# Kernel optimization log

Measured on AMD Instinct MI355X. Metric: run time of the kernel, lower is better.

The kernel has to match this reference:

```python
import jax, jax.numpy as jnp
import numpy as np

B, N = 4, 512
NF, EF = 12, 1          # node / edge feature dims (fixed in GraphClassifier)
QK = 128                # baseFeatNum -> QKDims = nValDims
NV_D, EV_D = 128, 32    # nValDims, eValDims
TR = 2 * NV_D           # Trans output = nValDims*2 = 256
NCLS = 5
EPS = 1e-5


def setup_inputs() -> dict:
    key = jax.random.key(0)
    ks = jax.random.split(key, 16)
    s = 0.1
    return {
        "nodes": jax.random.normal(ks[0], (B, N, NF), jnp.float32),
        "edges": jax.random.normal(ks[1], (B, N, N, EF), jnp.float32),
        "distances": jax.random.uniform(ks[2], (B, N, N), jnp.float32),
        "mask": jax.random.randint(ks[3], (B, N, N), 0, 2) > 0,
        "Wq": jax.random.normal(ks[4], (QK, NF), jnp.float32) * s,
        "bq": jnp.zeros((QK,), jnp.float32),
        "Wk": jax.random.normal(ks[5], (QK, NF), jnp.float32) * s,
        "bk": jnp.zeros((QK,), jnp.float32),
        "Wnv": jax.random.normal(ks[6], (NV_D, NF), jnp.float32) * s,
        "bnv": jnp.zeros((NV_D,), jnp.float32),
        "Wev": jax.random.normal(ks[7], (EV_D, EF), jnp.float32) * s,
        "bev": jnp.zeros((EV_D,), jnp.float32),
        "Wt": jax.random.normal(ks[8], (TR, NV_D + EV_D), jnp.float32) * s,
        "bt": jnp.zeros((TR,), jnp.float32),
        "gamma": jnp.ones((TR,), jnp.float32),
        "beta": jnp.zeros((TR,), jnp.float32),
        "Wc": jax.random.normal(ks[9], (NCLS, TR), jnp.float32) * s,
        "bc": jnp.zeros((NCLS,), jnp.float32),
    }


def reference(nodes, edges, distances, mask, Wq, bq, Wk, bk, Wnv, bnv,
              Wev, bev, Wt, bt, gamma, beta, Wc, bc):
    coeff = 1.0 / np.sqrt(QK).astype(np.float32)
    Q = nodes @ Wq.T + bq            # (b,N,QK)
    K = nodes @ Wk.T + bk            # (b,N,QK)
    NV = nodes @ Wnv.T + bnv         # (b,N,nValDims); NV[b,i,j]=NV_node[b,j] after repeat
    EV = edges @ Wev.T + bev         # (b,N,N,eValDims)

    dist_w = 1.0 / (distances + 1.0)
    scores = jnp.einsum('bik,bjk->bij', Q, K) * dist_w * coeff
    scores = jnp.where(mask, -jnp.inf, scores)
    w = jax.nn.softmax(scores, axis=-1)
    w = jnp.where(jnp.isnan(w), 0.0, w)  # fully-masked rows -> zero weights

    node_part = jnp.einsum('bij,bjd->bid', w, NV)     # weighted node values
    edge_part = jnp.einsum('bij,bijd->bid', w, EV)    # weighted edge values
    vals = jnp.concatenate([node_part, edge_part], axis=-1)
    vals = jnp.tanh(vals) @ Wt.T + bt                 # (b,N,2*nValDims)

    # BatchNorm1d in training mode: biased batch stats over (b*N)
    flat = vals.reshape(-1, TR)
    mu = flat.mean(axis=0)
    var = flat.var(axis=0)
    flat = (flat - mu) / jnp.sqrt(var + EPS) * gamma + beta
    vals = flat.reshape(vals.shape)

    return vals @ Wc.T + bc                           # (b,N,5)
```

## Files before the change

### kernel.cpp

```cpp
#include <hip/hip_runtime.h>
#include <math.h>

#define NNODE 512
#define NBATCH 4
#define NFEAT 12
#define QKD 128
#define NVD 128
#define EVD 32
#define CATD 160
#define CATB 168
#define TRD 256
#define NCLS 5
#define NROWS 2048
#define EPSV 1e-5f
#define NSTATBUF 8
#define NCHUNK 4
#define JC 128
#define RPB 8
#define SSW 132
#define KBW 136

typedef float floatx4 __attribute__((ext_vector_type(4)));
typedef __bf16 bf16x8 __attribute__((ext_vector_type(8)));
typedef unsigned short ushort_t;
typedef ushort_t ushort8 __attribute__((ext_vector_type(8)));
typedef ushort_t ushort4v __attribute__((ext_vector_type(4)));

static __device__ __forceinline__ ushort_t f2bf(float x) {
  unsigned int u = __float_as_uint(x);
  return (ushort_t)((u + 0x7fffu + ((u >> 16) & 1u)) >> 16);
}
static __device__ __forceinline__ bf16x8 pack8(ushort4v lo, ushort4v hi) {
  ushort8 u;
  u[0] = lo.x; u[1] = lo.y; u[2] = lo.z; u[3] = lo.w;
  u[4] = hi.x; u[5] = hi.y; u[6] = hi.z; u[7] = hi.w;
  return __builtin_bit_cast(bf16x8, u);
}

__global__ __launch_bounds__(256) void qkv_kernel(
    const float* __restrict__ nodes,
    const float* __restrict__ Wq, const float* __restrict__ bq,
    const float* __restrict__ Wk, const float* __restrict__ bk,
    const float* __restrict__ Wnv, const float* __restrict__ bnv,
    const float* __restrict__ Wt,
    ushort_t* __restrict__ Qb, ushort_t* __restrict__ Kb,
    ushort_t* __restrict__ NVT, ushort_t* __restrict__ Wtb,
    float* __restrict__ stats) {
  const int tid = threadIdx.x;
  const int blk = blockIdx.x;
  const int rowbase = blk * 8;
  const int b = rowbase >> 9;
  const int jloc = rowbase & (NNODE - 1);
  if (blk < 2 * NSTATBUF) stats[blk * 256 + tid] = 0.f;
  {
    const int base = blk * 160;
    if (tid < 160) Wtb[base + tid] = f2bf(Wt[base + tid]);
  }
  __shared__ float sn[RPB][NFEAT];
  if (tid < RPB * NFEAT) ((float*)sn)[tid] = nodes[(size_t)rowbase * NFEAT + tid];
  __syncthreads();

  {
    const int d  = tid & 127;
    const int rg = tid >> 7;
    float wq[NFEAT], wk[NFEAT];
#pragma unroll
    for (int k = 0; k < NFEAT; ++k) {
      wq[k] = Wq[d * NFEAT + k];
      wk[k] = Wk[d * NFEAT + k];
    }
    const float bqv = bq[d], bkv = bk[d];
#pragma unroll
    for (int rr = 0; rr < 4; ++rr) {
      const int rl = rg * 4 + rr;
      float aq = bqv, ak = bkv;
#pragma unroll
      for (int k = 0; k < NFEAT; ++k) {
        const float n = sn[rl][k];
        aq = fmaf(n, wq[k], aq);
        ak = fmaf(n, wk[k], ak);
      }
      Qb[(size_t)(rowbase + rl) * QKD + d] = f2bf(aq);
      Kb[(size_t)(rowbase + rl) * QKD + d] = f2bf(ak);
    }
  }
  {
    const int d    = tid >> 1;
    const int half = tid & 1;
    float wnv[NFEAT];
#pragma unroll
    for (int k = 0; k < NFEAT; ++k) wnv[k] = Wnv[d * NFEAT + k];
    const float bnvv = bnv[d];
    ushort4v v;
#pragma unroll
    for (int e = 0; e < 4; ++e) {
      const int rl = half * 4 + e;
      float av = bnvv;
#pragma unroll
      for (int k = 0; k < NFEAT; ++k) av = fmaf(sn[rl][k], wnv[k], av);
      v[e] = f2bf(av);
    }
    *(ushort4v*)(NVT + (size_t)b * QKD * NNODE + (size_t)d * NNODE +
                 jloc + half * 4) = v;
  }
}

__global__ __launch_bounds__(512) void attnTrans_kernel(
    const ushort_t* __restrict__ Qb, const ushort_t* __restrict__ Kb,
    const ushort_t* __restrict__ NVT,
    const float* __restrict__ edges, const float* __restrict__ dist,
    const int* __restrict__ mask,
    const float* __restrict__ Wev, const float* __restrict__ bev,
    const ushort_t* __restrict__ Wtb, const float* __restrict__ bt,
    float* __restrict__ vals, float* __restrict__ stats) {
  __shared__ ushort_t sKB[2][JC * KBW];
  __shared__ ushort_t sNV[2][QKD * KBW];
  __shared__ __align__(16) float sS[16][SSW];
  __shared__ ushort_t catb[RPB * CATB];
  __shared__ float sF[16], sF2[RPB], sSe[RPB], sSw[RPB];

  const int tid = threadIdx.x;
  const int bid = blockIdx.x;
  const int b   = bid >> 6;
  const int rg  = bid & 63;
  const int rowbase = b * NNODE + rg * RPB;

  const int lane = tid & 63;
  const int wv   = tid >> 6;
  const int col  = lane & 15;
  const int kg   = lane >> 4;

  if (tid < 16) sF[tid] = 0.f;

  const int jl  = wv * 16 + col;
  const int dpv = wv * 16 + col;
  const int sd   = tid >> 2;
  const int sseg = (tid & 3) * 32;

  float dd[NCHUNK][4]; int mm[NCHUNK][4];
  float ee0[NCHUNK], ee1[NCHUNK];
#pragma unroll
  for (int c = 0; c < NCHUNK; ++c) {
#pragma unroll
    for (int r = 0; r < 4; ++r) {
      const size_t off =
          (size_t)(rowbase + ((kg * 4 + r) & 7)) * NNODE + c * JC + jl;
      dd[c][r] = dist[off];
      mm[c][r] = mask[off];
    }
    ee0[c] = edges[(size_t)(rowbase + wv) * NNODE + c * JC + lane];
    ee1[c] = edges[(size_t)(rowbase + wv) * NNODE + c * JC + 64 + lane];
  }

  bf16x8 aq[4];
  {
    const ushort_t* Qr = Qb + (size_t)(rowbase + (col & 7)) * QKD;
#pragma unroll
    for (int ks = 0; ks < 4; ++ks)
      aq[ks] = pack8(*(const ushort4v*)(Qr + ks * 32 + kg * 4),
                     *(const ushort4v*)(Qr + ks * 32 + 16 + kg * 4));
  }

  ushort8 kreg[4], nreg[4];
  {
    const ushort8* ksrc =
        (const ushort8*)(Kb + (size_t)(b * NNODE + sd) * QKD + sseg);
    const ushort8* nsrc = (const ushort8*)(NVT + (size_t)b * QKD * NNODE +
                                           (size_t)sd * NNODE + sseg);
#pragma unroll
    for (int t = 0; t < 4; ++t) { kreg[t] = ksrc[t]; nreg[t] = nsrc[t]; }
  }

  float m_run = -__builtin_inff(), l_run = 0.f, se_run = 0.f;
  floatx4 acc = {0.f, 0.f, 0.f, 0.f};
  const float coeff = 0.0883883476483184f;

#pragma unroll
  for (int c = 0; c < NCHUNK; ++c) {
    {
      ushort8* kdst = (ushort8*)(&sKB[c & 1][0] + sd * KBW + sseg);
      ushort8* ndst = (ushort8*)(&sNV[c & 1][0] + sd * KBW + sseg);
#pragma unroll
      for (int t = 0; t < 4; ++t) { kdst[t] = kreg[t]; ndst[t] = nreg[t]; }
    }
    __syncthreads();

    if (c < NCHUNK - 1) {
      const int jb2 = (c + 1) * JC;
      const ushort8* ksrc =
          (const ushort8*)(Kb + (size_t)(b * NNODE + jb2 + sd) * QKD + sseg);
      const ushort8* nsrc = (const ushort8*)(NVT + (size_t)b * QKD * NNODE +
                                             (size_t)sd * NNODE + jb2 + sseg);
#pragma unroll
      for (int t = 0; t < 4; ++t) { kreg[t] = ksrc[t]; nreg[t] = nsrc[t]; }
    }

    {
      floatx4 sc = {0.f, 0.f, 0.f, 0.f};
      const ushort_t* kb = &sKB[c & 1][0] + (size_t)jl * KBW;
#pragma unroll
      for (int ks = 0; ks < 4; ++ks) {
        const bf16x8 bfk = pack8(*(const ushort4v*)(kb + ks * 32 + kg * 4),
                                 *(const ushort4v*)(kb + ks * 32 + 16 + kg * 4));
        sc = __builtin_amdgcn_mfma_f32_16x16x32_bf16(aq[ks], bfk, sc, 0, 0, 0);
      }
#pragma unroll
      for (int r = 0; r < 4; ++r) {
        float s = sc[r] * coeff / (dd[c][r] + 1.0f);
        if (mm[c][r]) s = -__builtin_inff();
        sS[kg * 4 + r][jl] = s;
      }
    }
    __syncthreads();

    {
      const float v0 = sS[wv][lane];
      const float v1 = sS[wv][lane + 64];
      float mc = fmaxf(v0, v1);
#pragma unroll
      for (int s = 1; s < 64; s <<= 1) mc = fmaxf(mc, __shfl_xor(mc, s, 64));
      const float mn = fmaxf(m_run, mc);
      const float f = (m_run > -__builtin_inff()) ? __expf(m_run - mn) : 0.f;
      float w0 = 0.f, w1 = 0.f;
      if (mn > -__builtin_inff()) {
        w0 = __expf(v0 - mn);
        w1 = __expf(v1 - mn);
      }
      sS[wv][lane]      = w0;
      sS[wv][lane + 64] = w1;
      float lc = w0 + w1;
      float sec = fmaf(w0, ee0[c], w1 * ee1[c]);
#pragma unroll
      for (int s = 1; s < 64; s <<= 1) {
        lc  += __shfl_xor(lc, s, 64);
        sec += __shfl_xor(sec, s, 64);
      }
      l_run  = l_run * f + lc;
      se_run = se_run * f + sec;
      m_run  = mn;
      if (lane == 0) sF[wv] = f;
    }
    __syncthreads();

    {
      acc[0] *= sF[kg * 4 + 0];
      acc[1] *= sF[kg * 4 + 1];
      acc[2] *= sF[kg * 4 + 2];
      acc[3] *= sF[kg * 4 + 3];
      const ushort_t* nv = &sNV[c & 1][0] + (size_t)dpv * KBW;
#pragma unroll
      for (int ks = 0; ks < 4; ++ks) {
        const float4 lo = *(const float4*)&sS[col][ks * 32 + kg * 4];
        const float4 hi = *(const float4*)&sS[col][ks * 32 + 16 + kg * 4];
        ushort8 u;
        u[0] = f2bf(lo.x); u[1] = f2bf(lo.y); u[2] = f2bf(lo.z); u[3] = f2bf(lo.w);
        u[4] = f2bf(hi.x); u[5] = f2bf(hi.y); u[6] = f2bf(hi.z); u[7] = f2bf(hi.w);
        const bf16x8 aw = __builtin_bit_cast(bf16x8, u);
        const bf16x8 bnv = pack8(*(const ushort4v*)(nv + ks * 32 + kg * 4),
                                 *(const ushort4v*)(nv + ks * 32 + 16 + kg * 4));
        acc = __builtin_amdgcn_mfma_f32_16x16x32_bf16(aw, bnv, acc, 0, 0, 0);
      }
    }
  }

  {
    const float inv = (l_run > 0.f) ? 1.f / l_run : 0.f;
    if (lane == 0) {
      sF2[wv] = inv;
      sSe[wv] = se_run * inv;
      sSw[wv] = (l_run > 0.f) ? 1.f : 0.f;
    }
  }
  __syncthreads();

  if (kg < 2) {
#pragma unroll
    for (int r = 0; r < 4; ++r) {
      const int row = kg * 4 + r;
      catb[row * CATB + dpv] = f2bf(tanhf(acc[r] * sF2[row]));
    }
  }
  if (tid < RPB * EVD) {
    const int r = tid >> 5, de = tid & 31;
    catb[r * CATB + NVD + de] =
        f2bf(tanhf(fmaf(Wev[de], sSe[r], bev[de] * sSw[r])));
  }
  __syncthreads();

  {
    bf16x8 af[5];
    const ushort_t* cr = catb + (size_t)(col & 7) * CATB;
#pragma unroll
    for (int ks = 0; ks < 5; ++ks)
      af[ks] = pack8(*(const ushort4v*)(cr + ks * 32 + kg * 4),
                     *(const ushort4v*)(cr + ks * 32 + 16 + kg * 4));
    float* sbuf = stats + (size_t)(bid & (NSTATBUF - 1)) * 2 * TRD;
#pragma unroll
    for (int t = 0; t < 2; ++t) {
      const int o = (wv * 2 + t) * 16 + col;
      const ushort_t* wr = Wtb + (size_t)o * CATD;
      floatx4 a2 = {0.f, 0.f, 0.f, 0.f};
#pragma unroll
      for (int ks = 0; ks < 5; ++ks) {
        const bf16x8 bf = pack8(*(const ushort4v*)(wr + ks * 32 + kg * 4),
                                *(const ushort4v*)(wr + ks * 32 + 16 + kg * 4));
        a2 = __builtin_amdgcn_mfma_f32_16x16x32_bf16(af[ks], bf, a2, 0, 0, 0);
      }
      const float bto = bt[o];
      float s1 = 0.f, s2 = 0.f;
#pragma unroll
      for (int r = 0; r < 4; ++r) {
        const float v2 = a2[r] + bto;
        if (kg < 2) {
          vals[(size_t)(rowbase + kg * 4 + r) * TRD + o] = v2;
          s1 += v2;
          s2 = fmaf(v2, v2, s2);
        }
      }
      s1 += __shfl_xor(s1, 16, 64); s2 += __shfl_xor(s2, 16, 64);
      s1 += __shfl_xor(s1, 32, 64); s2 += __shfl_xor(s2, 32, 64);
      if (kg == 0) {
        atomicAdd(&sbuf[o], s1);
        atomicAdd(&sbuf[TRD + o], s2);
      }
    }
  }
}

__global__ __launch_bounds__(256) void outbn_kernel(
    const float* __restrict__ vals, const float* __restrict__ stats,
    const float* __restrict__ gamma, const float* __restrict__ beta,
    const float* __restrict__ Wc, const float* __restrict__ bc,
    float* __restrict__ out) {
  __shared__ float sW[NCLS][TRD];
  __shared__ float sb[NCLS];
  __shared__ float red[4][NCLS];
  const int tid = threadIdx.x;
  const int o = tid;
  float s1 = 0.f, s2 = 0.f;
#pragma unroll
  for (int k = 0; k < NSTATBUF; ++k) {
    s1 += stats[k * 2 * TRD + o];
    s2 += stats[k * 2 * TRD + TRD + o];
  }
  const float invN = 1.0f / (float)NROWS;
  const float mu  = s1 * invN;
  const float var = s2 * invN - mu * mu;
  const float inv = 1.0f / sqrtf(var + EPSV);
  const float g = gamma[o] * inv;
  const float bterm = beta[o] - mu * g;
  float v[NCLS];
#pragma unroll
  for (int c = 0; c < NCLS; ++c) {
    const float wc = Wc[c * TRD + o];
    sW[c][o] = wc * g;
    v[c] = wc * bterm;
  }
#pragma unroll
  for (int s = 1; s < 64; s <<= 1) {
#pragma unroll
    for (int c = 0; c < NCLS; ++c) v[c] += __shfl_xor(v[c], s, 64);
  }
  if ((tid & 63) == 0) {
#pragma unroll
    for (int c = 0; c < NCLS; ++c) red[tid >> 6][c] = v[c];
  }
  __syncthreads();
  if (tid < NCLS)
    sb[tid] = bc[tid] + red[0][tid] + red[1][tid] + red[2][tid] + red[3][tid];
  __syncthreads();

  const int lane = tid & 63;
  const int row = blockIdx.x * 4 + (tid >> 6);
  float vv[TRD / 64];
#pragma unroll
  for (int t = 0; t < TRD / 64; ++t)
    vv[t] = vals[(size_t)row * TRD + lane + 64 * t];
#pragma unroll
  for (int c = 0; c < NCLS; ++c) {
    float p = 0.f;
#pragma unroll
    for (int t = 0; t < TRD / 64; ++t)
      p = fmaf(vv[t], sW[c][lane + 64 * t], p);
#pragma unroll
    for (int s = 1; s < 64; s <<= 1) p += __shfl_xor(p, s, 64);
    if (lane == 0) out[(size_t)row * NCLS + c] = p + sb[c];
  }
}

extern "C" void kernel_launch(void* const* d_in, const int* in_sizes, int n_in,
                              void* d_out, int out_size, void* d_ws, size_t ws_size,
                              hipStream_t stream) {
  (void)in_sizes; (void)n_in; (void)out_size; (void)ws_size;
  const float* nodes = (const float*)d_in[0];
  const float* edges = (const float*)d_in[1];
  const float* dist  = (const float*)d_in[2];
  const int*   mask  = (const int*)d_in[3];
  const float* Wq  = (const float*)d_in[4];
  const float* bq  = (const float*)d_in[5];
  const float* Wk  = (const float*)d_in[6];
  const float* bk  = (const float*)d_in[7];
  const float* Wnv = (const float*)d_in[8];
  const float* bnv = (const float*)d_in[9];
  const float* Wev = (const float*)d_in[10];
  const float* bev = (const float*)d_in[11];
  const float* Wt  = (const float*)d_in[12];
  const float* bt  = (const float*)d_in[13];
  const float* gamma = (const float*)d_in[14];
  const float* beta  = (const float*)d_in[15];
  const float* Wc  = (const float*)d_in[16];
  const float* bc  = (const float*)d_in[17];

  char* w = (char*)d_ws;
  ushort_t* Qb  = (ushort_t*)w;                w += (size_t)NROWS * QKD * 2;
  ushort_t* Kb  = (ushort_t*)w;                w += (size_t)NROWS * QKD * 2;
  ushort_t* NVT = (ushort_t*)w;                w += (size_t)NBATCH * QKD * NNODE * 2;
  ushort_t* Wtb = (ushort_t*)w;                w += (size_t)TRD * CATD * 2;
  float* vals  = (float*)w;                    w += (size_t)NROWS * TRD * 4;
  float* stats = (float*)w;
  float* outp  = (float*)d_out;

  qkv_kernel<<<NROWS / RPB, 256, 0, stream>>>(nodes, Wq, bq, Wk, bk, Wnv, bnv,
                                              Wt, Qb, Kb, NVT, Wtb, stats);
  attnTrans_kernel<<<NROWS / RPB, 512, 0, stream>>>(
      Qb, Kb, NVT, edges, dist, mask, Wev, bev, Wtb, bt, vals, stats);
  outbn_kernel<<<NROWS / 4, 256, 0, stream>>>(vals, stats, gamma, beta,
                                              Wc, bc, outp);
}
```

Before: 34.47 us.

## Permute K-dim layout for direct MFMA fragment loads, drop LDS staging of K/NV

```diff
diff --git a/kernel.cpp b/kernel.cpp
--- a/kernel.cpp
+++ b/kernel.cpp
@@ -18,23 +18,22 @@
 #define JC 128
 #define RPB 8
 #define SSW 132
-#define KBW 136
+#define WBW 136
 
 typedef float floatx4 __attribute__((ext_vector_type(4)));
 typedef __bf16 bf16x8 __attribute__((ext_vector_type(8)));
 typedef unsigned short ushort_t;
-typedef ushort_t ushort8 __attribute__((ext_vector_type(8)));
 typedef ushort_t ushort4v __attribute__((ext_vector_type(4)));
 
 static __device__ __forceinline__ ushort_t f2bf(float x) {
   unsigned int u = __float_as_uint(x);
   return (ushort_t)((u + 0x7fffu + ((u >> 16) & 1u)) >> 16);
 }
-static __device__ __forceinline__ bf16x8 pack8(ushort4v lo, ushort4v hi) {
-  ushort8 u;
-  u[0] = lo.x; u[1] = lo.y; u[2] = lo.z; u[3] = lo.w;
-  u[4] = hi.x; u[5] = hi.y; u[6] = hi.z; u[7] = hi.w;
-  return __builtin_bit_cast(bf16x8, u);
+static __device__ __forceinline__ int slot32(int r) {
+  return ((r & 15) >> 2) * 8 + (r & 3) + ((r >> 4) << 2);
+}
+static __device__ __forceinline__ int kslot(int k) {
+  return (k & ~31) + slot32(k & 31);
 }
 
 __global__ __launch_bounds__(256) void qkv_kernel(
@@ -52,10 +51,8 @@
   const int b = rowbase >> 9;
   const int jloc = rowbase & (NNODE - 1);
   if (blk < 2 * NSTATBUF) stats[blk * 256 + tid] = 0.f;
-  {
-    const int base = blk * 160;
-    if (tid < 160) Wtb[base + tid] = f2bf(Wt[base + tid]);
-  }
+  if (tid < CATD)
+    Wtb[(size_t)blk * CATD + kslot(tid)] = f2bf(Wt[(size_t)blk * CATD + tid]);
   __shared__ float sn[RPB][NFEAT];
   if (tid < RPB * NFEAT) ((float*)sn)[tid] = nodes[(size_t)rowbase * NFEAT + tid];
   __syncthreads();
@@ -63,6 +60,7 @@
   {
     const int d  = tid & 127;
     const int rg = tid >> 7;
+    const int sd = kslot(d);
     float wq[NFEAT], wk[NFEAT];
 #pragma unroll
     for (int k = 0; k < NFEAT; ++k) {
@@ -80,8 +78,8 @@
         aq = fmaf(n, wq[k], aq);
         ak = fmaf(n, wk[k], ak);
       }
-      Qb[(size_t)(rowbase + rl) * QKD + d] = f2bf(aq);
-      Kb[(size_t)(rowbase + rl) * QKD + d] = f2bf(ak);
+      Qb[(size_t)(rowbase + rl) * QKD + sd] = f2bf(aq);
+      Kb[(size_t)(rowbase + rl) * QKD + sd] = f2bf(ak);
     }
   }
   {
@@ -100,8 +98,9 @@
       for (int k = 0; k < NFEAT; ++k) av = fmaf(sn[rl][k], wnv[k], av);
       v[e] = f2bf(av);
     }
-    *(ushort4v*)(NVT + (size_t)b * QKD * NNODE + (size_t)d * NNODE +
-                 jloc + half * 4) = v;
+    const int js = jloc + half * 4;
+    const int jsl = (js & ~31) + slot32(js & 31);
+    *(ushort4v*)(NVT + (size_t)b * QKD * NNODE + (size_t)d * NNODE + jsl) = v;
   }
 }
 
@@ -113,10 +112,9 @@
     const float* __restrict__ Wev, const float* __restrict__ bev,
     const ushort_t* __restrict__ Wtb, const float* __restrict__ bt,
     float* __restrict__ vals, float* __restrict__ stats) {
-  __shared__ ushort_t sKB[2][JC * KBW];
-  __shared__ ushort_t sNV[2][QKD * KBW];
-  __shared__ __align__(16) float sS[16][SSW];
-  __shared__ ushort_t catb[RPB * CATB];
+  __shared__ __align__(16) float sS[2][RPB][SSW];
+  __shared__ __align__(16) ushort_t sWb[2][16][WBW];
+  __shared__ __align__(16) ushort_t catb[RPB * CATB];
   __shared__ float sF[16], sF2[RPB], sSe[RPB], sSw[RPB];
 
   const int tid = threadIdx.x;
@@ -134,41 +132,34 @@
 
   const int jl  = wv * 16 + col;
   const int dpv = wv * 16 + col;
-  const int sd   = tid >> 2;
-  const int sseg = (tid & 3) * 32;
-
-  float dd[NCHUNK][4]; int mm[NCHUNK][4];
-  float ee0[NCHUNK], ee1[NCHUNK];
-#pragma unroll
-  for (int c = 0; c < NCHUNK; ++c) {
+
+  bf16x8 aq[4];
+  {
+    const ushort_t* Qr = Qb + (size_t)(rowbase + (col & 7)) * QKD;
+#pragma unroll
+    for (int ks = 0; ks < 4; ++ks)
+      aq[ks] = *(const bf16x8*)(Qr + ks * 32 + kg * 8);
+  }
+
+  bf16x8 kf[2][4], nf[2][4];
+  float dd[2][4]; int mm[2][4];
+  float ee0[2], ee1[2];
+  {
+    const ushort_t* Kr = Kb + (size_t)(b * NNODE + jl) * QKD;
+    const ushort_t* Nr = NVT + ((size_t)b * QKD + dpv) * NNODE;
+#pragma unroll
+    for (int ks = 0; ks < 4; ++ks) {
+      kf[0][ks] = *(const bf16x8*)(Kr + ks * 32 + kg * 8);
+      nf[0][ks] = *(const bf16x8*)(Nr + ks * 32 + kg * 8);
+    }
 #pragma unroll
     for (int r = 0; r < 4; ++r) {
-      const size_t off =
-          (size_t)(rowbase + ((kg * 4 + r) & 7)) * NNODE + c * JC + jl;
-      dd[c][r] = dist[off];
-      mm[c][r] = mask[off];
-    }
-    ee0[c] = edges[(size_t)(rowbase + wv) * NNODE + c * JC + lane];
-    ee1[c] = edges[(size_t)(rowbase + wv) * NNODE + c * JC + 64 + lane];
-  }
-
-  bf16x8 aq[4];
-  {
-    const ushort_t* Qr = Qb + (size_t)(rowbase + (col & 7)) * QKD;
-#pragma unroll
-    for (int ks = 0; ks < 4; ++ks)
-      aq[ks] = pack8(*(const ushort4v*)(Qr + ks * 32 + kg * 4),
-                     *(const ushort4v*)(Qr + ks * 32 + 16 + kg * 4));
-  }
-
-  ushort8 kreg[4], nreg[4];
-  {
-    const ushort8* ksrc =
-        (const ushort8*)(Kb + (size_t)(b * NNODE + sd) * QKD + sseg);
-    const ushort8* nsrc = (const ushort8*)(NVT + (size_t)b * QKD * NNODE +
-                                           (size_t)sd * NNODE + sseg);
-#pragma unroll
-    for (int t = 0; t < 4; ++t) { kreg[t] = ksrc[t]; nreg[t] = nsrc[t]; }
+      const size_t off = (size_t)(rowbase + ((kg * 4 + r) & 7)) * NNODE + jl;
+      dd[0][r] = dist[off];
+      mm[0][r] = mask[off];
+    }
+    ee0[0] = edges[(size_t)(rowbase + wv) * NNODE + lane];
+    ee1[0] = edges[(size_t)(rowbase + wv) * NNODE + 64 + lane];
   }
 
   float m_run = -__builtin_inff(), l_run = 0.f, se_run = 0.f;
@@ -177,45 +168,47 @@
 
 #pragma unroll
   for (int c = 0; c < NCHUNK; ++c) {
-    {
-      ushort8* kdst = (ushort8*)(&sKB[c & 1][0] + sd * KBW + sseg);
-      ushort8* ndst = (ushort8*)(&sNV[c & 1][0] + sd * KBW + sseg);
-#pragma unroll
-      for (int t = 0; t < 4; ++t) { kdst[t] = kreg[t]; ndst[t] = nreg[t]; }
-    }
-    __syncthreads();
-
-    if (c < NCHUNK - 1) {
+    const int cur = c & 1, nxt = (c + 1) & 1;
+    if (c + 1 < NCHUNK) {
       const int jb2 = (c + 1) * JC;
-      const ushort8* ksrc =
-          (const ushort8*)(Kb + (size_t)(b * NNODE + jb2 + sd) * QKD + sseg);
-      const ushort8* nsrc = (const ushort8*)(NVT + (size_t)b * QKD * NNODE +
-                                             (size_t)sd * NNODE + jb2 + sseg);
-#pragma unroll
-      for (int t = 0; t < 4; ++t) { kreg[t] = ksrc[t]; nreg[t] = nsrc[t]; }
+      const ushort_t* Kr = Kb + (size_t)(b * NNODE + jb2 + jl) * QKD;
+      const ushort_t* Nr = NVT + ((size_t)b * QKD + dpv) * NNODE + jb2;
+#pragma unroll
+      for (int ks = 0; ks < 4; ++ks) {
+        kf[nxt][ks] = *(const bf16x8*)(Kr + ks * 32 + kg * 8);
+        nf[nxt][ks] = *(const bf16x8*)(Nr + ks * 32 + kg * 8);
+      }
+#pragma unroll
+      for (int r = 0; r < 4; ++r) {
+        const size_t off =
+            (size_t)(rowbase + ((kg * 4 + r) & 7)) * NNODE + jb2 + jl;
+        dd[nxt][r] = dist[off];
+        mm[nxt][r] = mask[off];
+      }
+      ee0[nxt] = edges[(size_t)(rowbase + wv) * NNODE + jb2 + lane];
+      ee1[nxt] = edges[(size_t)(rowbase + wv) * NNODE + jb2 + 64 + lane];
     }
 
     {
       floatx4 sc = {0.f, 0.f, 0.f, 0.f};
-      const ushort_t* kb = &sKB[c & 1][0] + (size_t)jl * KBW;
-#pragma unroll
-      for (int ks = 0; ks < 4; ++ks) {
-        const bf16x8 bfk = pack8(*(const ushort4v*)(kb + ks * 32 + kg * 4),
-                                 *(const ushort4v*)(kb + ks * 32 + 16 + kg * 4));
-        sc = __builtin_amdgcn_mfma_f32_16x16x32_bf16(aq[ks], bfk, sc, 0, 0, 0);
-      }
-#pragma unroll
-      for (int r = 0; r < 4; ++r) {
-        float s = sc[r] * coeff / (dd[c][r] + 1.0f);
-        if (mm[c][r]) s = -__builtin_inff();
-        sS[kg * 4 + r][jl] = s;
+#pragma unroll
+      for (int ks = 0; ks < 4; ++ks)
+        sc = __builtin_amdgcn_mfma_f32_16x16x32_bf16(aq[ks], kf[cur][ks], sc,
+                                                     0, 0, 0);
+      if (kg < 2) {
+#pragma unroll
+        for (int r = 0; r < 4; ++r) {
+          float s = sc[r] * coeff / (dd[cur][r] + 1.0f);
+          if (mm[cur][r]) s = -__builtin_inff();
+          sS[cur][kg * 4 + r][jl] = s;
+        }
       }
     }
     __syncthreads();
 
     {
-      const float v0 = sS[wv][lane];
-      const float v1 = sS[wv][lane + 64];
+      const float v0 = sS[cur][wv][lane];
+      const float v1 = sS[cur][wv][lane + 64];
       float mc = fmaxf(v0, v1);
 #pragma unroll
       for (int s = 1; s < 64; s <<= 1) mc = fmaxf(mc, __shfl_xor(mc, s, 64));
@@ -226,10 +219,11 @@
         w0 = __expf(v0 - mn);
         w1 = __expf(v1 - mn);
       }
-      sS[wv][lane]      = w0;
-      sS[wv][lane + 64] = w1;
+      const int j0 = lane, j1 = lane + 64;
+      sWb[cur][wv][(j0 & ~31) + slot32(j0 & 31)] = f2bf(w0);
+      sWb[cur][wv][(j1 & ~31) + slot32(j1 & 31)] = f2bf(w1);
       float lc = w0 + w1;
-      float sec = fmaf(w0, ee0[c], w1 * ee1[c]);
+      float sec = fmaf(w0, ee0[cur], w1 * ee1[cur]);
 #pragma unroll
       for (int s = 1; s < 64; s <<= 1) {
         lc  += __shfl_xor(lc, s, 64);
@@ -247,18 +241,12 @@
       acc[1] *= sF[kg * 4 + 1];
       acc[2] *= sF[kg * 4 + 2];
       acc[3] *= sF[kg * 4 + 3];
-      const ushort_t* nv = &sNV[c & 1][0] + (size_t)dpv * KBW;
 #pragma unroll
       for (int ks = 0; ks < 4; ++ks) {
-        const float4 lo = *(const float4*)&sS[col][ks * 32 + kg * 4];
-        const float4 hi = *(const float4*)&sS[col][ks * 32 + 16 + kg * 4];
-        ushort8 u;
-        u[0] = f2bf(lo.x); u[1] = f2bf(lo.y); u[2] = f2bf(lo.z); u[3] = f2bf(lo.w);
-        u[4] = f2bf(hi.x); u[5] = f2bf(hi.y); u[6] = f2bf(hi.z); u[7] = f2bf(hi.w);
-        const bf16x8 aw = __builtin_bit_cast(bf16x8, u);
-        const bf16x8 bnv = pack8(*(const ushort4v*)(nv + ks * 32 + kg * 4),
-                                 *(const ushort4v*)(nv + ks * 32 + 16 + kg * 4));
-        acc = __builtin_amdgcn_mfma_f32_16x16x32_bf16(aw, bnv, acc, 0, 0, 0);
+        const bf16x8 aw =
+            *(const bf16x8*)(&sWb[cur][col][ks * 32 + kg * 8]);
+        acc = __builtin_amdgcn_mfma_f32_16x16x32_bf16(aw, nf[cur][ks], acc,
+                                                      0, 0, 0);
       }
     }
   }
@@ -277,12 +265,12 @@
 #pragma unroll
     for (int r = 0; r < 4; ++r) {
       const int row = kg * 4 + r;
-      catb[row * CATB + dpv] = f2bf(tanhf(acc[r] * sF2[row]));
+      catb[row * CATB + kslot(dpv)] = f2bf(tanhf(acc[r] * sF2[row]));
     }
   }
   if (tid < RPB * EVD) {
     const int r = tid >> 5, de = tid & 31;
-    catb[r * CATB + NVD + de] =
+    catb[r * CATB + 128 + slot32(de)] =
         f2bf(tanhf(fmaf(Wev[de], sSe[r], bev[de] * sSw[r])));
   }
   __syncthreads();
@@ -292,8 +280,7 @@
     const ushort_t* cr = catb + (size_t)(col & 7) * CATB;
 #pragma unroll
     for (int ks = 0; ks < 5; ++ks)
-      af[ks] = pack8(*(const ushort4v*)(cr + ks * 32 + kg * 4),
-                     *(const ushort4v*)(cr + ks * 32 + 16 + kg * 4));
+      af[ks] = *(const bf16x8*)(cr + ks * 32 + kg * 8);
     float* sbuf = stats + (size_t)(bid & (NSTATBUF - 1)) * 2 * TRD;
 #pragma unroll
     for (int t = 0; t < 2; ++t) {
@@ -302,8 +289,7 @@
       floatx4 a2 = {0.f, 0.f, 0.f, 0.f};
 #pragma unroll
       for (int ks = 0; ks < 5; ++ks) {
-        const bf16x8 bf = pack8(*(const ushort4v*)(wr + ks * 32 + kg * 4),
-                                *(const ushort4v*)(wr + ks * 32 + 16 + kg * 4));
+        const bf16x8 bf = *(const bf16x8*)(wr + ks * 32 + kg * 8);
         a2 = __builtin_amdgcn_mfma_f32_16x16x32_bf16(af[ks], bf, a2, 0, 0, 0);
       }
       const float bto = bt[o];
```

Result: faster. 31.91 us (-7.4%).
